# Kernel optimization log

Measured on AMD Instinct MI355X. Metric: run time of the kernel, lower is better.

The kernel has to match this reference:

```python
import jax, jax.numpy as jnp
import numpy as np

# --- model hyperparameters (from init_kwargs) ---
DIM = 2048
INTER = 1408          # moe_inter_dim
E = 16                # n_routed_experts
TOPK = 4              # n_activated_experts
G = 4                 # n_expert_groups
TOPK_G = 2            # n_limited_groups
N_SHARED = 2
ROUTE_SCALE = 1.0
INIT_STD = 0.02
B, S = 1, 2048


def setup_inputs() -> dict:
    key = jax.random.key(0)
    ks = jax.random.split(key, 9)
    std = INIT_STD
    x = jax.random.normal(ks[0], (B, S, DIM), jnp.float32)
    gate_w = jax.random.normal(ks[1], (E, DIM), jnp.float32) * std
    expert_bias = jnp.zeros((E,), jnp.float32)
    # stacked expert SwiGLU weights; torch Linear(in,out) -> stored here as [in,out]
    w1 = jax.random.normal(ks[2], (E, DIM, INTER), jnp.float32) * std
    w3 = jax.random.normal(ks[3], (E, DIM, INTER), jnp.float32) * std
    w2 = jax.random.normal(ks[4], (E, INTER, DIM), jnp.float32) * std
    # shared experts MLP (inter = n_shared_experts * moe_inter_dim)
    sh = N_SHARED * INTER
    sw1 = jax.random.normal(ks[5], (DIM, sh), jnp.float32) * std
    sw3 = jax.random.normal(ks[6], (DIM, sh), jnp.float32) * std
    sw2 = jax.random.normal(ks[7], (sh, DIM), jnp.float32) * std
    return {"x": x, "gate_w": gate_w, "expert_bias": expert_bias,
            "w1": w1, "w2": w2, "w3": w3,
            "sw1": sw1, "sw2": sw2, "sw3": sw3}


def reference(x, gate_w, expert_bias, w1, w2, w3, sw1, sw2, sw3):
    b, s, d = x.shape
    T = b * s
    xf = x.reshape(T, d)

    # ---- Gate ----
    scores = jax.nn.sigmoid(xf @ gate_w.T)          # [T, E] (score_function='sigmoid')
    original_scores = scores
    scores = scores + expert_bias
    # grouped routing: keep top-k groups, mask the rest to -inf
    sg = scores.reshape(T, G, E // G)
    group_scores = sg.max(axis=-1)                   # [T, G]
    _, gidx = jax.lax.top_k(group_scores, TOPK_G)    # [T, TOPK_G]
    gmask = jnp.zeros((T, G), bool).at[jnp.arange(T)[:, None], gidx].set(True)
    masked = jnp.where(gmask[:, :, None], sg, -jnp.inf).reshape(T, E)
    _, idx = jax.lax.top_k(masked, TOPK)             # [T, TOPK] expert indices
    w = jnp.take_along_axis(original_scores, idx, axis=1)
    w = w / jnp.sum(w, axis=-1, keepdims=True)       # sigmoid path normalization
    w = w * ROUTE_SCALE

    # dense combine weights: zero for non-selected experts -> exact same math
    cw = jnp.zeros((T, E), x.dtype).at[jnp.arange(T)[:, None], idx].add(w)

    # ---- routed experts (stacked SwiGLU) ----
    h = jax.nn.silu(jnp.einsum('td,edh->teh', xf, w1)) * jnp.einsum('td,edh->teh', xf, w3)
    y = jnp.einsum('teh,ehd,te->td', h, w2, cw)

    # ---- shared experts ----
    z = (jax.nn.silu(xf @ sw1) * (xf @ sw3)) @ sw2

    return (y + z).reshape(b, s, d)
```

## Files before the change

kernel.cpp:

```cpp
#include <hip/hip_runtime.h>
#include <hip/hip_bf16.h>

#define T_     2048
#define DIM_   2048
#define INTER_ 1408
#define SH_    2816
#define E_     16
#define TOPK_  4

typedef short bf16x8 __attribute__((ext_vector_type(8)));
typedef short bf16x4 __attribute__((ext_vector_type(4)));
typedef float f32x4  __attribute__((ext_vector_type(4)));

__device__ __forceinline__ short f2bf(float f) {
    unsigned u = __builtin_bit_cast(unsigned, f);
    u = (u + 0x7fffu + ((u >> 16) & 1u)) >> 16;
    return (short)u;
}
__device__ __forceinline__ float bf2f(short s) {
    unsigned u = ((unsigned)(unsigned short)s) << 16;
    return __builtin_bit_cast(float, u);
}
__device__ __forceinline__ f32x4 mfma16(bf16x8 a, bf16x8 b, f32x4 c) {
    return __builtin_amdgcn_mfma_f32_16x16x32_bf16(a, b, c, 0, 0, 0);
}

#define LDK 48
__device__ __forceinline__ int soff(int r, int slot) {
    return r * LDK + ((slot ^ ((r >> 2) & 3)) << 3);
}
__device__ __forceinline__ int qoff(int r, int slot) {
    return r * 32 + ((slot ^ ((r >> 1) & 3)) << 3);
}

__device__ __forceinline__ void async_copy16(short* lds, const short* g) {
#if defined(__has_builtin) && __has_builtin(__builtin_amdgcn_global_load_lds)
    __builtin_amdgcn_global_load_lds(
        (const __attribute__((address_space(1))) void*)g,
        (__attribute__((address_space(3))) void*)lds, 16, 0, 0);
#else
    *(bf16x8*)((char*)lds + (size_t)(threadIdx.x & 63) * 16) = *(const bf16x8*)g;
#endif
}

__device__ __forceinline__ bf16x8 pack44(float4 a, float4 b) {
    bf16x8 r;
    r[0] = f2bf(a.x); r[1] = f2bf(a.y); r[2] = f2bf(a.z); r[3] = f2bf(a.w);
    r[4] = f2bf(b.x); r[5] = f2bf(b.y); r[6] = f2bf(b.z); r[7] = f2bf(b.w);
    return r;
}

__global__ void zero_counts_kernel(int* __restrict__ counts) {
    if (threadIdx.x < E_) counts[threadIdx.x] = 0;
}

__global__ void transpose_bf16_kernel(const float* __restrict__ src,
                                      short* __restrict__ dst,
                                      int K, int N) {
    src += (size_t)blockIdx.z * K * N;
    dst += (size_t)blockIdx.z * N * K;
    int n0 = blockIdx.x * 64, k0 = blockIdx.y * 64;
    __shared__ short tile[64][66];
    int t = threadIdx.x;
    int hi = t >> 4;
    int c4 = (t & 15) << 2;
#pragma unroll
    for (int i = 0; i < 4; ++i) {
        int k = i * 16 + hi;
        float4 v = *(const float4*)(src + (size_t)(k0 + k) * N + n0 + c4);
        tile[k][c4 + 0] = f2bf(v.x);
        tile[k][c4 + 1] = f2bf(v.y);
        tile[k][c4 + 2] = f2bf(v.z);
        tile[k][c4 + 3] = f2bf(v.w);
    }
    __syncthreads();
#pragma unroll
    for (int i = 0; i < 4; ++i) {
        int n = i * 16 + hi;
        bf16x4 o;
        o[0] = tile[c4 + 0][n];
        o[1] = tile[c4 + 1][n];
        o[2] = tile[c4 + 2][n];
        o[3] = tile[c4 + 3][n];
        *(bf16x4*)(dst + (size_t)(n0 + n) * K + k0 + c4) = o;
    }
}

__global__ void gate_kernel(const float* __restrict__ X,
                            const float* __restrict__ GW,
                            const float* __restrict__ BIAS,
                            int*   __restrict__ counts,
                            int*   __restrict__ ltok,
                            int*   __restrict__ lslot,
                            float* __restrict__ lwt,
                            float* __restrict__ aw) {
    int t = blockIdx.x;
    int lane = threadIdx.x;
    const float* xp = X + (size_t)t * DIM_;
    float acc[E_];
#pragma unroll
    for (int e = 0; e < E_; ++e) acc[e] = 0.f;
    for (int d = lane; d < DIM_; d += 64) {
        float xv = xp[d];
#pragma unroll
        for (int e = 0; e < E_; ++e) acc[e] += xv * GW[e * DIM_ + d];
    }
#pragma unroll
    for (int off = 32; off > 0; off >>= 1) {
#pragma unroll
        for (int e = 0; e < E_; ++e) acc[e] += __shfl_down(acc[e], off, 64);
    }
    if (lane == 0) {
        float orig[E_], s[E_];
#pragma unroll
        for (int e = 0; e < E_; ++e) {
            float sg = 1.f / (1.f + expf(-acc[e]));
            orig[e] = sg;
            s[e] = sg + BIAS[e];
        }
        float gs[4];
#pragma unroll
        for (int g = 0; g < 4; ++g)
            gs[g] = fmaxf(fmaxf(s[4*g], s[4*g+1]), fmaxf(s[4*g+2], s[4*g+3]));
        int g0 = 0;
#pragma unroll
        for (int g = 1; g < 4; ++g) if (gs[g] > gs[g0]) g0 = g;
        int g1 = -1;
#pragma unroll
        for (int g = 0; g < 4; ++g)
            if (g != g0 && (g1 < 0 || gs[g] > gs[g1])) g1 = g;
        unsigned allow = (0xFu << (g0 * 4)) | (0xFu << (g1 * 4));
        unsigned taken = 0;
        int sel[TOPK_]; float wv[TOPK_]; float wsum = 0.f;
#pragma unroll
        for (int k = 0; k < TOPK_; ++k) {
            int bi = -1; float bv = 0.f;
#pragma unroll
            for (int e = 0; e < E_; ++e) {
                if (((allow >> e) & 1u) && !((taken >> e) & 1u)) {
                    if (bi < 0 || s[e] > bv) { bi = e; bv = s[e]; }
                }
            }
            taken |= 1u << bi;
            sel[k] = bi; wv[k] = orig[bi]; wsum += orig[bi];
        }
        float inv = 1.0f / wsum;
#pragma unroll
        for (int k = 0; k < TOPK_; ++k) {
            int e = sel[k];
            float w = wv[k] * inv;
            int pos = atomicAdd(&counts[e], 1);
            ltok [e * T_ + pos] = t;
            lslot[e * T_ + pos] = t * TOPK_ + k;
            lwt  [e * T_ + pos] = w;
            aw[t * TOPK_ + k] = w;
        }
    }
}

template<bool GATHER, bool BF16W>
__launch_bounds__(256, 2)
__global__ void swiglu_gemm(const float* __restrict__ X,
                            const void* __restrict__ W1g,
                            const void* __restrict__ W3g,
                            short* __restrict__ Hout,
                            int N, int K,
                            const int* __restrict__ counts,
                            const int* __restrict__ ltok,
                            const int* __restrict__ lslot) {
    int e = GATHER ? blockIdx.z : 0;
    int cnt = GATHER ? counts[e] : (int)(gridDim.y * 128);
    int row_base = blockIdx.y * 128;
    if (row_base >= cnt) return;
    int bn0 = blockIdx.x * 128;

    __shared__ __align__(16) short As [128 * LDK];
    __shared__ __align__(16) short Bs1[128 * LDK];
    __shared__ __align__(16) short Bs3[128 * LDK];

    int t = threadIdx.x;
    int ar = t >> 1, ah = t & 1;
    int arow = row_base + ar;
    bool avalid; int atok;
    if (GATHER) { avalid = arow < cnt; atok = avalid ? ltok[e * T_ + arow] : 0; }
    else        { avalid = true;       atok = arow; }
    const float* aptr = X + (size_t)atok * DIM_ + ah * 16;

    int l = t & 63, wv = t >> 6;
    int wm = (wv >> 1) << 6, wn = (wv & 1) << 6;
    int lr = l & 15, lk = l >> 4;

    const short* bSrc1[2]; const short* bSrc3[2];
    const float* Wf1 = nullptr; const float* Wf3 = nullptr;
    if constexpr (BF16W) {
        const short* Wb1 = (const short*)W1g + (size_t)e * N * K;
        const short* Wb3 = (const short*)W3g + (size_t)e * N * K;
        int r_ = l >> 2, sp = l & 3;
#pragma unroll
        for (int c = 0; c < 2; ++c) {
            int chunk = c * 4 + wv;
            int r = chunk * 16 + r_;
            int ss = sp ^ ((r >> 1) & 3);
            bSrc1[c] = Wb1 + (size_t)(bn0 + r) * K + ss * 8;
            bSrc3[c] = Wb3 + (size_t)(bn0 + r) * K + ss * 8;
        }
    } else {
        Wf1 = (const float*)W1g + (size_t)e * K * N;
        Wf3 = (const float*)W3g + (size_t)e * K * N;
    }

    f32x4 acc1[4][4], acc3[4][4];
    f32x4 z4 = {0.f, 0.f, 0.f, 0.f};
#pragma unroll
    for (int i = 0; i < 4; ++i)
#pragma unroll
        for (int j = 0; j < 4; ++j) { acc1[i][j] = z4; acc3[i][j] = z4; }

    for (int k0 = 0; k0 < K; k0 += 32) {
        float4 v0, v1, v2, v3;
        if (avalid) {
            const float4* p = (const float4*)(aptr + k0);
            v0 = p[0]; v1 = p[1]; v2 = p[2]; v3 = p[3];
        } else {
            v0 = v1 = v2 = v3 = make_float4(0.f, 0.f, 0.f, 0.f);
        }
        *(bf16x8*)&As[soff(ar, ah * 2)]     = pack44(v0, v1);
        *(bf16x8*)&As[soff(ar, ah * 2 + 1)] = pack44(v2, v3);
        if constexpr (BF16W) {
#pragma unroll
            for (int c = 0; c < 2; ++c) {
                int chunk = c * 4 + wv;
                async_copy16(&Bs1[chunk * 512], bSrc1[c] + k0);
                async_copy16(&Bs3[chunk * 512], bSrc3[c] + k0);
            }
        } else {
            for (int it = t; it < 512; it += 256) {
                int n = it & 127, kc = it >> 7;
                const float* b1p = Wf1 + (size_t)(k0 + kc * 8) * N + bn0 + n;
                const float* b3p = Wf3 + (size_t)(k0 + kc * 8) * N + bn0 + n;
                bf16x8 p1, p3;
#pragma unroll
                for (int j = 0; j < 8; ++j) {
                    p1[j] = f2bf(b1p[(size_t)j * N]);
                    p3[j] = f2bf(b3p[(size_t)j * N]);
                }
                *(bf16x8*)&Bs1[soff(n, kc)] = p1;
                *(bf16x8*)&Bs3[soff(n, kc)] = p3;
            }
        }
        __syncthreads();
        bf16x8 af[4], b1f[4], b3f[4];
#pragma unroll
        for (int mf = 0; mf < 4; ++mf)
            af[mf] = *(const bf16x8*)&As[soff(wm + mf * 16 + lr, lk)];
#pragma unroll
        for (int nf = 0; nf < 4; ++nf) {
            int n = wn + nf * 16 + lr;
            if constexpr (BF16W) {
                b1f[nf] = *(const bf16x8*)&Bs1[qoff(n, lk)];
                b3f[nf] = *(const bf16x8*)&Bs3[qoff(n, lk)];
            } else {
                b1f[nf] = *(const bf16x8*)&Bs1[soff(n, lk)];
                b3f[nf] = *(const bf16x8*)&Bs3[soff(n, lk)];
            }
        }
#pragma unroll
        for (int mf = 0; mf < 4; ++mf)
#pragma unroll
            for (int nf = 0; nf < 4; ++nf) {
                acc1[mf][nf] = mfma16(af[mf], b1f[nf], acc1[mf][nf]);
                acc3[mf][nf] = mfma16(af[mf], b3f[nf], acc3[mf][nf]);
            }
        __syncthreads();
    }
#pragma unroll
    for (int mf = 0; mf < 4; ++mf)
#pragma unroll
        for (int nf = 0; nf < 4; ++nf)
#pragma unroll
            for (int j = 0; j < 4; ++j) {
                float a1 = acc1[mf][nf][j];
                float a3 = acc3[mf][nf][j];
                float hv = a1 / (1.f + __expf(-a1)) * a3;
                int r = wm + mf * 16 + lk * 4 + j;
                int gr = row_base + r;
                int col = bn0 + wn + nf * 16 + lr;
                if (!GATHER || gr < cnt) {
                    size_t orow = GATHER ? (size_t)lslot[(size_t)e * T_ + gr]
                                         : (size_t)gr;
                    Hout[orow * (size_t)N + col] = f2bf(hv);
                }
            }
}

template<bool ROUTED, bool BF16W>
__launch_bounds__(256, 2)
__global__ void out_gemm(const short* __restrict__ Hg,
                         const void* __restrict__ W2g,
                         float* __restrict__ Out,
                         short* __restrict__ Obuf,
                         int K, int use_obuf,
                         const int* __restrict__ counts,
                         const int* __restrict__ lslot,
                         const float* __restrict__ lwt) {
    int e = ROUTED ? blockIdx.z : 0;
    int cnt = ROUTED ? counts[e] : T_;
    int row_base = blockIdx.y * 128;
    if (row_base >= cnt) return;
    int bn0 = blockIdx.x * 128;

    __shared__ __align__(16) short As[128 * LDK];
    __shared__ __align__(16) short Bs[128 * LDK];

    int t = threadIdx.x;
    int l = t & 63, wv = t >> 6;
    int wm = (wv >> 1) << 6, wn = (wv & 1) << 6;
    int lr = l & 15, lk = l >> 4;

    const short* aSrc[2]; const short* bSrc[2];
    const float* Wf2 = nullptr;
    const short* aptr = nullptr; bool avalid = true; int ar = 0, ah = 0;
    if constexpr (BF16W) {
        const short* Wb2 = (const short*)W2g + (size_t)e * (size_t)DIM_ * K;
        int r_ = l >> 2, sp = l & 3;
#pragma unroll
        for (int c = 0; c < 2; ++c) {
            int chunk = c * 4 + wv;
            int r = chunk * 16 + r_;
            int ss = sp ^ ((r >> 1) & 3);
            size_t hrow;
            if constexpr (ROUTED) {
                int gr = row_base + r;
                hrow = (size_t)((gr < cnt) ? lslot[(size_t)e * T_ + gr] : 0);
            } else {
                hrow = (size_t)(row_base + r);
            }
            aSrc[c] = Hg + hrow * K + ss * 8;
            bSrc[c] = Wb2 + (size_t)(bn0 + r) * K + ss * 8;
        }
    } else {
        Wf2 = (const float*)W2g + (size_t)e * K * DIM_;
        ar = t >> 1; ah = t & 1;
        int arow = row_base + ar;
        if constexpr (ROUTED) {
            avalid = arow < cnt;
            aptr = avalid ? Hg + (size_t)lslot[(size_t)e * T_ + arow] * K + ah * 16 : Hg;
        } else {
            aptr = Hg + (size_t)arow * K + ah * 16;
        }
    }

    f32x4 acc[4][4];
    f32x4 z4 = {0.f, 0.f, 0.f, 0.f};
#pragma unroll
    for (int i = 0; i < 4; ++i)
#pragma unroll
        for (int j = 0; j < 4; ++j) acc[i][j] = z4;

    for (int k0 = 0; k0 < K; k0 += 32) {
        if constexpr (BF16W) {
#pragma unroll
            for (int c = 0; c < 2; ++c) {
                int chunk = c * 4 + wv;
                async_copy16(&As[chunk * 512], aSrc[c] + k0);
                async_copy16(&Bs[chunk * 512], bSrc[c] + k0);
            }
        } else {
            bf16x8 pa0, pa1;
            if (avalid) {
                pa0 = *(const bf16x8*)(aptr + k0);
                pa1 = *(const bf16x8*)(aptr + k0 + 8);
            } else {
#pragma unroll
                for (int j = 0; j < 8; ++j) { pa0[j] = 0; pa1[j] = 0; }
            }
            *(bf16x8*)&As[soff(ar, ah * 2)]     = pa0;
            *(bf16x8*)&As[soff(ar, ah * 2 + 1)] = pa1;
            for (int it = t; it < 512; it += 256) {
                int n = it & 127, kc = it >> 7;
                const float* bp = Wf2 + (size_t)(k0 + kc * 8) * DIM_ + bn0 + n;
                bf16x8 p;
#pragma unroll
                for (int j = 0; j < 8; ++j) p[j] = f2bf(bp[(size_t)j * DIM_]);
                *(bf16x8*)&Bs[soff(n, kc)] = p;
            }
        }
        __syncthreads();
        bf16x8 af[4], bfr[4];
#pragma unroll
        for (int mf = 0; mf < 4; ++mf) {
            int r = wm + mf * 16 + lr;
            if constexpr (BF16W) af[mf] = *(const bf16x8*)&As[qoff(r, lk)];
            else                 af[mf] = *(const bf16x8*)&As[soff(r, lk)];
        }
#pragma unroll
        for (int nf = 0; nf < 4; ++nf) {
            int n = wn + nf * 16 + lr;
            if constexpr (BF16W) bfr[nf] = *(const bf16x8*)&Bs[qoff(n, lk)];
            else                 bfr[nf] = *(const bf16x8*)&Bs[soff(n, lk)];
        }
#pragma unroll
        for (int mf = 0; mf < 4; ++mf)
#pragma unroll
            for (int nf = 0; nf < 4; ++nf)
                acc[mf][nf] = mfma16(af[mf], bfr[nf], acc[mf][nf]);
        __syncthreads();
    }
#pragma unroll
    for (int mf = 0; mf < 4; ++mf)
#pragma unroll
        for (int nf = 0; nf < 4; ++nf)
#pragma unroll
            for (int j = 0; j < 4; ++j) {
                float v = acc[mf][nf][j];
                int r = wm + mf * 16 + lk * 4 + j;
                int gr = row_base + r;
                int col = bn0 + wn + nf * 16 + lr;
                if constexpr (ROUTED) {
                    if (gr < cnt) {
                        int a = lslot[(size_t)e * T_ + gr];
                        if (use_obuf) {
                            Obuf[(size_t)a * DIM_ + col] = f2bf(v);
                        } else {
                            float w = lwt[(size_t)e * T_ + gr];
                            atomicAdd(&Out[(size_t)(a >> 2) * DIM_ + col], v * w);
                        }
                    }
                } else {
                    Out[(size_t)gr * DIM_ + col] = v;
                }
            }
}

__global__ void combine_kernel(const short* __restrict__ Obuf,
                               const float* __restrict__ aw,
                               float* __restrict__ Out) {
    int t = blockIdx.x;
    int c0 = threadIdx.x << 3;
    float s[8];
#pragma unroll
    for (int j = 0; j < 8; ++j) s[j] = 0.f;
#pragma unroll
    for (int k = 0; k < TOPK_; ++k) {
        float w = aw[t * TOPK_ + k];
        const short* rp = Obuf + ((size_t)(t * TOPK_ + k)) * DIM_ + c0;
#pragma unroll
        for (int j = 0; j < 8; ++j) s[j] += w * bf2f(rp[j]);
    }
    float* op = Out + (size_t)t * DIM_ + c0;
#pragma unroll
    for (int j = 0; j < 8; ++j) op[j] += s[j];
}

extern "C" void kernel_launch(void* const* d_in, const int* in_sizes, int n_in,
                              void* d_out, int out_size, void* d_ws, size_t ws_size,
                              hipStream_t stream) {
    const float* x     = (const float*)d_in[0];
    const float* gw    = (const float*)d_in[1];
    const float* ebias = (const float*)d_in[2];
    const float* w1    = (const float*)d_in[3];
    const float* w2    = (const float*)d_in[4];
    const float* w3    = (const float*)d_in[5];
    const float* sw1   = (const float*)d_in[6];
    const float* sw2   = (const float*)d_in[7];
    const float* sw3   = (const float*)d_in[8];
    float* out = (float*)d_out;

    char* wsb = (char*)d_ws;
    int*   counts = (int*)wsb;
    int*   ltok   = (int*)(wsb + 1024);
    int*   lslot  = (int*)(wsb + 1024 + 131072);
    float* lwt    = (float*)(wsb + 1024 + 2 * 131072);
    float* aw     = (float*)(wsb + 1024 + 3 * 131072);
    size_t off = 1024 + 3 * 131072 + 32768;
    short* hbuf = (short*)(wsb + off);
    size_t hbuf_sz = (size_t)T_ * TOPK_ * INTER_ * 2;
    size_t obuf_sz = (size_t)T_ * TOPK_ * DIM_ * 2;
    size_t hs_sz   = (size_t)T_ * SH_ * 2;
    size_t wt_sz   = (size_t)E_ * INTER_ * DIM_ * 2;
    size_t swt_sz  = (size_t)SH_ * DIM_ * 2;

    size_t need_fp32a = off + hbuf_sz + hs_sz;
    size_t need_fp32  = need_fp32a + obuf_sz;
    size_t need_bf16  = need_fp32 + 3 * wt_sz + 3 * swt_sz;

    size_t o2 = off + hbuf_sz;
    short* obuf = (short*)(wsb + o2);
    int use_obuf = (ws_size >= need_fp32) ? 1 : 0;
    if (use_obuf) o2 += obuf_sz;
    short* hs = (short*)(wsb + o2); o2 += hs_sz;
    short* wt1  = (short*)(wsb + o2); o2 += wt_sz;
    short* wt3  = (short*)(wsb + o2); o2 += wt_sz;
    short* wt2  = (short*)(wsb + o2); o2 += wt_sz;
    short* swt1 = (short*)(wsb + o2); o2 += swt_sz;
    short* swt3 = (short*)(wsb + o2); o2 += swt_sz;
    short* swt2 = (short*)(wsb + o2);
    int bf16w = (ws_size >= need_bf16) ? 1 : 0;

    zero_counts_kernel<<<1, 64, 0, stream>>>(counts);
    gate_kernel<<<T_, 64, 0, stream>>>(x, gw, ebias, counts, ltok, lslot, lwt, aw);

    if (bf16w) {
        transpose_bf16_kernel<<<dim3(INTER_/64, DIM_/64, E_), 256, 0, stream>>>(w1, wt1, DIM_, INTER_);
        transpose_bf16_kernel<<<dim3(INTER_/64, DIM_/64, E_), 256, 0, stream>>>(w3, wt3, DIM_, INTER_);
        transpose_bf16_kernel<<<dim3(DIM_/64, INTER_/64, E_), 256, 0, stream>>>(w2, wt2, INTER_, DIM_);
        transpose_bf16_kernel<<<dim3(SH_/64, DIM_/64, 1), 256, 0, stream>>>(sw1, swt1, DIM_, SH_);
        transpose_bf16_kernel<<<dim3(SH_/64, DIM_/64, 1), 256, 0, stream>>>(sw3, swt3, DIM_, SH_);
        transpose_bf16_kernel<<<dim3(DIM_/64, SH_/64, 1), 256, 0, stream>>>(sw2, swt2, SH_, DIM_);

        swiglu_gemm<false, true><<<dim3(SH_/128, T_/128), 256, 0, stream>>>(
            x, swt1, swt3, hs, SH_, DIM_, nullptr, nullptr, nullptr);
        out_gemm<false, true><<<dim3(DIM_/128, T_/128), 256, 0, stream>>>(
            hs, swt2, out, nullptr, SH_, 0, nullptr, nullptr, nullptr);
        swiglu_gemm<true, true><<<dim3(INTER_/128, T_/128, E_), 256, 0, stream>>>(
            x, wt1, wt3, hbuf, INTER_, DIM_, counts, ltok, lslot);
        out_gemm<true, true><<<dim3(DIM_/128, T_/128, E_), 256, 0, stream>>>(
            hbuf, wt2, out, obuf, INTER_, 1, counts, lslot, lwt);
        combine_kernel<<<T_, 256, 0, stream>>>(obuf, aw, out);
    } else {
        swiglu_gemm<false, false><<<dim3(SH_/128, T_/128), 256, 0, stream>>>(
            x, sw1, sw3, hs, SH_, DIM_, nullptr, nullptr, nullptr);
        out_gemm<false, false><<<dim3(DIM_/128, T_/128), 256, 0, stream>>>(
            hs, sw2, out, nullptr, SH_, 0, nullptr, nullptr, nullptr);
        swiglu_gemm<true, false><<<dim3(INTER_/128, T_/128, E_), 256, 0, stream>>>(
            x, w1, w3, hbuf, INTER_, DIM_, counts, ltok, lslot);
        out_gemm<true, false><<<dim3(DIM_/128, T_/128, E_), 256, 0, stream>>>(
            hbuf, w2, out, obuf, INTER_, use_obuf, counts, lslot, lwt);
        if (use_obuf)
            combine_kernel<<<T_, 256, 0, stream>>>(obuf, aw, out);
    }
}
```

Before: 1.218 ms.

## Pre-convert activations to bf16, double-buffer async GEMM loads, fuse combine into shared GEMM

A separate kernel now converts x to bf16 once, so the SwiGLU GEMMs load A tiles with async global-to-LDS copies the same way they load weights. Both GEMMs now use double-buffered LDS with prefetch of the next K tile, which removes one barrier per iteration. The routed top-k combine moves into the shared-expert output GEMM epilogue, which drops combine_kernel and the read-modify-write of out. Other changes: the fp32-weight fallback path is removed, the transpose writes 16-byte vectors, out_gemm launch bounds go from 2 to 3, and the launches are reordered. The trade-off is that the code now always assumes a large enough workspace, and the larger LDS footprint may reduce occupancy.

```diff
diff --git a/kernel.cpp b/kernel.cpp
--- a/kernel.cpp
+++ b/kernel.cpp
@@ -24,25 +24,6 @@
 __device__ __forceinline__ f32x4 mfma16(bf16x8 a, bf16x8 b, f32x4 c) {
     return __builtin_amdgcn_mfma_f32_16x16x32_bf16(a, b, c, 0, 0, 0);
 }
-
-#define LDK 48
-__device__ __forceinline__ int soff(int r, int slot) {
-    return r * LDK + ((slot ^ ((r >> 2) & 3)) << 3);
-}
-__device__ __forceinline__ int qoff(int r, int slot) {
-    return r * 32 + ((slot ^ ((r >> 1) & 3)) << 3);
-}
-
-__device__ __forceinline__ void async_copy16(short* lds, const short* g) {
-#if defined(__has_builtin) && __has_builtin(__builtin_amdgcn_global_load_lds)
-    __builtin_amdgcn_global_load_lds(
-        (const __attribute__((address_space(1))) void*)g,
-        (__attribute__((address_space(3))) void*)lds, 16, 0, 0);
-#else
-    *(bf16x8*)((char*)lds + (size_t)(threadIdx.x & 63) * 16) = *(const bf16x8*)g;
-#endif
-}
-
 __device__ __forceinline__ bf16x8 pack44(float4 a, float4 b) {
     bf16x8 r;
     r[0] = f2bf(a.x); r[1] = f2bf(a.y); r[2] = f2bf(a.z); r[3] = f2bf(a.w);
@@ -50,8 +31,25 @@
     return r;
 }
 
+__device__ __forceinline__ int qoff(int r, int slot) {
+    return r * 32 + ((slot ^ ((r >> 1) & 3)) << 3);
+}
+
+__device__ __forceinline__ void async_copy16(short* lds, const short* g) {
+    __builtin_amdgcn_global_load_lds(
+        (const __attribute__((address_space(1))) void*)g,
+        (__attribute__((address_space(3))) void*)lds, 16, 0, 0);
+}
+
 __global__ void zero_counts_kernel(int* __restrict__ counts) {
     if (threadIdx.x < E_) counts[threadIdx.x] = 0;
+}
+
+__global__ void xconv_kernel(const float* __restrict__ x, short* __restrict__ xb) {
+    size_t i = ((size_t)blockIdx.x * 256 + threadIdx.x) * 8;
+    float4 a = *(const float4*)(x + i);
+    float4 b = *(const float4*)(x + i + 4);
+    *(bf16x8*)(xb + i) = pack44(a, b);
 }
 
 __global__ void transpose_bf16_kernel(const float* __restrict__ src,
@@ -74,15 +72,14 @@
         tile[k][c4 + 3] = f2bf(v.w);
     }
     __syncthreads();
-#pragma unroll
-    for (int i = 0; i < 4; ++i) {
-        int n = i * 16 + hi;
-        bf16x4 o;
-        o[0] = tile[c4 + 0][n];
-        o[1] = tile[c4 + 1][n];
-        o[2] = tile[c4 + 2][n];
-        o[3] = tile[c4 + 3][n];
-        *(bf16x4*)(dst + (size_t)(n0 + n) * K + k0 + c4) = o;
+    int n_ = t >> 3, kg = t & 7;
+#pragma unroll
+    for (int p = 0; p < 2; ++p) {
+        int n = p * 32 + n_;
+        bf16x8 o;
+#pragma unroll
+        for (int j = 0; j < 8; ++j) o[j] = tile[kg * 8 + j][n];
+        *(bf16x8*)(dst + (size_t)(n0 + n) * K + k0 + kg * 8) = o;
     }
 }
 
@@ -158,55 +155,48 @@
     }
 }
 
-template<bool GATHER, bool BF16W>
+template<bool GATHER>
 __launch_bounds__(256, 2)
-__global__ void swiglu_gemm(const float* __restrict__ X,
-                            const void* __restrict__ W1g,
-                            const void* __restrict__ W3g,
-                            short* __restrict__ Hout,
-                            int N, int K,
-                            const int* __restrict__ counts,
-                            const int* __restrict__ ltok,
-                            const int* __restrict__ lslot) {
+__global__ void swiglu_gemm2(const short* __restrict__ Xb,
+                             const short* __restrict__ W1g,
+                             const short* __restrict__ W3g,
+                             short* __restrict__ Hout,
+                             int N, int K,
+                             const int* __restrict__ counts,
+                             const int* __restrict__ ltok,
+                             const int* __restrict__ lslot) {
     int e = GATHER ? blockIdx.z : 0;
     int cnt = GATHER ? counts[e] : (int)(gridDim.y * 128);
     int row_base = blockIdx.y * 128;
     if (row_base >= cnt) return;
     int bn0 = blockIdx.x * 128;
-
-    __shared__ __align__(16) short As [128 * LDK];
-    __shared__ __align__(16) short Bs1[128 * LDK];
-    __shared__ __align__(16) short Bs3[128 * LDK];
-
-    int t = threadIdx.x;
-    int ar = t >> 1, ah = t & 1;
-    int arow = row_base + ar;
-    bool avalid; int atok;
-    if (GATHER) { avalid = arow < cnt; atok = avalid ? ltok[e * T_ + arow] : 0; }
-    else        { avalid = true;       atok = arow; }
-    const float* aptr = X + (size_t)atok * DIM_ + ah * 16;
-
-    int l = t & 63, wv = t >> 6;
+    const short* W1 = W1g + (size_t)e * N * K;
+    const short* W3 = W3g + (size_t)e * N * K;
+
+    __shared__ __align__(16) short As [2][4096];
+    __shared__ __align__(16) short Bs1[2][4096];
+    __shared__ __align__(16) short Bs3[2][4096];
+
+    int t = threadIdx.x, l = t & 63, wv = t >> 6;
     int wm = (wv >> 1) << 6, wn = (wv & 1) << 6;
     int lr = l & 15, lk = l >> 4;
-
-    const short* bSrc1[2]; const short* bSrc3[2];
-    const float* Wf1 = nullptr; const float* Wf3 = nullptr;
-    if constexpr (BF16W) {
-        const short* Wb1 = (const short*)W1g + (size_t)e * N * K;
-        const short* Wb3 = (const short*)W3g + (size_t)e * N * K;
-        int r_ = l >> 2, sp = l & 3;
-#pragma unroll
-        for (int c = 0; c < 2; ++c) {
-            int chunk = c * 4 + wv;
-            int r = chunk * 16 + r_;
-            int ss = sp ^ ((r >> 1) & 3);
-            bSrc1[c] = Wb1 + (size_t)(bn0 + r) * K + ss * 8;
-            bSrc3[c] = Wb3 + (size_t)(bn0 + r) * K + ss * 8;
-        }
-    } else {
-        Wf1 = (const float*)W1g + (size_t)e * K * N;
-        Wf3 = (const float*)W3g + (size_t)e * K * N;
+    int r_ = l >> 2, sp = l & 3;
+
+    const short *aS[2], *b1S[2], *b3S[2];
+#pragma unroll
+    for (int c = 0; c < 2; ++c) {
+        int chunk = c * 4 + wv;
+        int r = chunk * 16 + r_;
+        int ss = sp ^ ((r >> 1) & 3);
+        int grow = row_base + r;
+        int tok;
+        if constexpr (GATHER) {
+            int ci = grow < cnt ? grow : cnt - 1;
+            tok = ltok[e * T_ + ci];
+        } else tok = grow;
+        aS [c] = Xb + (size_t)tok * K + ss * 8;
+        b1S[c] = W1 + (size_t)(bn0 + r) * K + ss * 8;
+        b3S[c] = W3 + (size_t)(bn0 + r) * K + ss * 8;
     }
 
     f32x4 acc1[4][4], acc3[4][4];
@@ -216,53 +206,36 @@
 #pragma unroll
         for (int j = 0; j < 4; ++j) { acc1[i][j] = z4; acc3[i][j] = z4; }
 
-    for (int k0 = 0; k0 < K; k0 += 32) {
-        float4 v0, v1, v2, v3;
-        if (avalid) {
-            const float4* p = (const float4*)(aptr + k0);
-            v0 = p[0]; v1 = p[1]; v2 = p[2]; v3 = p[3];
-        } else {
-            v0 = v1 = v2 = v3 = make_float4(0.f, 0.f, 0.f, 0.f);
-        }
-        *(bf16x8*)&As[soff(ar, ah * 2)]     = pack44(v0, v1);
-        *(bf16x8*)&As[soff(ar, ah * 2 + 1)] = pack44(v2, v3);
-        if constexpr (BF16W) {
+    int nt = K >> 5;
+#pragma unroll
+    for (int c = 0; c < 2; ++c) {
+        int chunk = c * 4 + wv;
+        async_copy16(&As [0][chunk * 512], aS [c]);
+        async_copy16(&Bs1[0][chunk * 512], b1S[c]);
+        async_copy16(&Bs3[0][chunk * 512], b3S[c]);
+    }
+    __syncthreads();
+    int cur = 0;
+    for (int kt = 0; kt < nt; ++kt) {
+        if (kt + 1 < nt) {
+            int k0 = (kt + 1) << 5;
 #pragma unroll
             for (int c = 0; c < 2; ++c) {
                 int chunk = c * 4 + wv;
-                async_copy16(&Bs1[chunk * 512], bSrc1[c] + k0);
-                async_copy16(&Bs3[chunk * 512], bSrc3[c] + k0);
-            }
-        } else {
-            for (int it = t; it < 512; it += 256) {
-                int n = it & 127, kc = it >> 7;
-                const float* b1p = Wf1 + (size_t)(k0 + kc * 8) * N + bn0 + n;
-                const float* b3p = Wf3 + (size_t)(k0 + kc * 8) * N + bn0 + n;
-                bf16x8 p1, p3;
-#pragma unroll
-                for (int j = 0; j < 8; ++j) {
-                    p1[j] = f2bf(b1p[(size_t)j * N]);
-                    p3[j] = f2bf(b3p[(size_t)j * N]);
-                }
-                *(bf16x8*)&Bs1[soff(n, kc)] = p1;
-                *(bf16x8*)&Bs3[soff(n, kc)] = p3;
-            }
-        }
-        __syncthreads();
+                async_copy16(&As [cur ^ 1][chunk * 512], aS [c] + k0);
+                async_copy16(&Bs1[cur ^ 1][chunk * 512], b1S[c] + k0);
+                async_copy16(&Bs3[cur ^ 1][chunk * 512], b3S[c] + k0);
+            }
+        }
         bf16x8 af[4], b1f[4], b3f[4];
 #pragma unroll
         for (int mf = 0; mf < 4; ++mf)
-            af[mf] = *(const bf16x8*)&As[soff(wm + mf * 16 + lr, lk)];
+            af[mf] = *(const bf16x8*)&As[cur][qoff(wm + mf * 16 + lr, lk)];
 #pragma unroll
         for (int nf = 0; nf < 4; ++nf) {
             int n = wn + nf * 16 + lr;
-            if constexpr (BF16W) {
-                b1f[nf] = *(const bf16x8*)&Bs1[qoff(n, lk)];
-                b3f[nf] = *(const bf16x8*)&Bs3[qoff(n, lk)];
-            } else {
-                b1f[nf] = *(const bf16x8*)&Bs1[soff(n, lk)];
-                b3f[nf] = *(const bf16x8*)&Bs3[soff(n, lk)];
-            }
+            b1f[nf] = *(const bf16x8*)&Bs1[cur][qoff(n, lk)];
+            b3f[nf] = *(const bf16x8*)&Bs3[cur][qoff(n, lk)];
         }
 #pragma unroll
         for (int mf = 0; mf < 4; ++mf)
@@ -272,6 +245,7 @@
                 acc3[mf][nf] = mfma16(af[mf], b3f[nf], acc3[mf][nf]);
             }
         __syncthreads();
+        cur ^= 1;
     }
 #pragma unroll
     for (int mf = 0; mf < 4; ++mf)
@@ -293,61 +267,47 @@
             }
 }
 
-template<bool ROUTED, bool BF16W>
-__launch_bounds__(256, 2)
-__global__ void out_gemm(const short* __restrict__ Hg,
-                         const void* __restrict__ W2g,
-                         float* __restrict__ Out,
-                         short* __restrict__ Obuf,
-                         int K, int use_obuf,
-                         const int* __restrict__ counts,
-                         const int* __restrict__ lslot,
-                         const float* __restrict__ lwt) {
+template<bool ROUTED, bool COMBINE>
+__launch_bounds__(256, 3)
+__global__ void out_gemm2(const short* __restrict__ Hg,
+                          const short* __restrict__ W2g,
+                          float* __restrict__ Out,
+                          short* __restrict__ Obuf,
+                          const float* __restrict__ aw,
+                          int K,
+                          const int* __restrict__ counts,
+                          const int* __restrict__ lslot) {
     int e = ROUTED ? blockIdx.z : 0;
     int cnt = ROUTED ? counts[e] : T_;
     int row_base = blockIdx.y * 128;
     if (row_base >= cnt) return;
     int bn0 = blockIdx.x * 128;
-
-    __shared__ __align__(16) short As[128 * LDK];
-    __shared__ __align__(16) short Bs[128 * LDK];
-
-    int t = threadIdx.x;
-    int l = t & 63, wv = t >> 6;
+    const short* W2 = W2g + (size_t)e * (size_t)DIM_ * K;
+
+    __shared__ __align__(16) short As[2][4096];
+    __shared__ __align__(16) short Bs[2][4096];
+
+    int t = threadIdx.x, l = t & 63, wv = t >> 6;
     int wm = (wv >> 1) << 6, wn = (wv & 1) << 6;
     int lr = l & 15, lk = l >> 4;
-
-    const short* aSrc[2]; const short* bSrc[2];
-    const float* Wf2 = nullptr;
-    const short* aptr = nullptr; bool avalid = true; int ar = 0, ah = 0;
-    if constexpr (BF16W) {
-        const short* Wb2 = (const short*)W2g + (size_t)e * (size_t)DIM_ * K;
-        int r_ = l >> 2, sp = l & 3;
-#pragma unroll
-        for (int c = 0; c < 2; ++c) {
-            int chunk = c * 4 + wv;
-            int r = chunk * 16 + r_;
-            int ss = sp ^ ((r >> 1) & 3);
-            size_t hrow;
-            if constexpr (ROUTED) {
-                int gr = row_base + r;
-                hrow = (size_t)((gr < cnt) ? lslot[(size_t)e * T_ + gr] : 0);
-            } else {
-                hrow = (size_t)(row_base + r);
-            }
-            aSrc[c] = Hg + hrow * K + ss * 8;
-            bSrc[c] = Wb2 + (size_t)(bn0 + r) * K + ss * 8;
-        }
-    } else {
-        Wf2 = (const float*)W2g + (size_t)e * K * DIM_;
-        ar = t >> 1; ah = t & 1;
-        int arow = row_base + ar;
+    int r_ = l >> 2, sp = l & 3;
+
+    const short *aS[2], *bS[2];
+#pragma unroll
+    for (int c = 0; c < 2; ++c) {
+        int chunk = c * 4 + wv;
+        int r = chunk * 16 + r_;
+        int ss = sp ^ ((r >> 1) & 3);
+        size_t hrow;
         if constexpr (ROUTED) {
-            avalid = arow < cnt;
-            aptr = avalid ? Hg + (size_t)lslot[(size_t)e * T_ + arow] * K + ah * 16 : Hg;
+            int grow = row_base + r;
+            int ci = grow < cnt ? grow : cnt - 1;
+            hrow = (size_t)lslot[(size_t)e * T_ + ci];
         } else {
-            aptr = Hg + (size_t)arow * K + ah * 16;
-        }
+            hrow = (size_t)(row_base + r);
+        }
+        aS[c] = Hg + hrow * K + ss * 8;
+        bS[c] = W2 + (size_t)(bn0 + r) * K + ss * 8;
     }
 
     f32x4 acc[4][4];
@@ -357,54 +317,39 @@
 #pragma unroll
         for (int j = 0; j < 4; ++j) acc[i][j] = z4;
 
-    for (int k0 = 0; k0 < K; k0 += 32) {
-        if constexpr (BF16W) {
+    int nt = K >> 5;
+#pragma unroll
+    for (int c = 0; c < 2; ++c) {
+        int chunk = c * 4 + wv;
+        async_copy16(&As[0][chunk * 512], aS[c]);
+        async_copy16(&Bs[0][chunk * 512], bS[c]);
+    }
+    __syncthreads();
+    int cur = 0;
+    for (int kt = 0; kt < nt; ++kt) {
+        if (kt + 1 < nt) {
+            int k0 = (kt + 1) << 5;
 #pragma unroll
             for (int c = 0; c < 2; ++c) {
                 int chunk = c * 4 + wv;
-                async_copy16(&As[chunk * 512], aSrc[c] + k0);
-                async_copy16(&Bs[chunk * 512], bSrc[c] + k0);
-            }
-        } else {
-            bf16x8 pa0, pa1;
-            if (avalid) {
-                pa0 = *(const bf16x8*)(aptr + k0);
-                pa1 = *(const bf16x8*)(aptr + k0 + 8);
-            } else {
-#pragma unroll
-                for (int j = 0; j < 8; ++j) { pa0[j] = 0; pa1[j] = 0; }
-            }
-            *(bf16x8*)&As[soff(ar, ah * 2)]     = pa0;
-            *(bf16x8*)&As[soff(ar, ah * 2 + 1)] = pa1;
-            for (int it = t; it < 512; it += 256) {
-                int n = it & 127, kc = it >> 7;
-                const float* bp = Wf2 + (size_t)(k0 + kc * 8) * DIM_ + bn0 + n;
-                bf16x8 p;
-#pragma unroll
-                for (int j = 0; j < 8; ++j) p[j] = f2bf(bp[(size_t)j * DIM_]);
-                *(bf16x8*)&Bs[soff(n, kc)] = p;
-            }
-        }
-        __syncthreads();
+                async_copy16(&As[cur ^ 1][chunk * 512], aS[c] + k0);
+                async_copy16(&Bs[cur ^ 1][chunk * 512], bS[c] + k0);
+            }
+        }
         bf16x8 af[4], bfr[4];
 #pragma unroll
-        for (int mf = 0; mf < 4; ++mf) {
-            int r = wm + mf * 16 + lr;
-            if constexpr (BF16W) af[mf] = *(const bf16x8*)&As[qoff(r, lk)];
-            else                 af[mf] = *(const bf16x8*)&As[soff(r, lk)];
-        }
-#pragma unroll
-        for (int nf = 0; nf < 4; ++nf) {
-            int n = wn + nf * 16 + lr;
-            if constexpr (BF16W) bfr[nf] = *(const bf16x8*)&Bs[qoff(n, lk)];
-            else                 bfr[nf] = *(const bf16x8*)&Bs[soff(n, lk)];
-        }
+        for (int mf = 0; mf < 4; ++mf)
+            af[mf] = *(const bf16x8*)&As[cur][qoff(wm + mf * 16 + lr, lk)];
+#pragma unroll
+        for (int nf = 0; nf < 4; ++nf)
+            bfr[nf] = *(const bf16x8*)&Bs[cur][qoff(wn + nf * 16 + lr, lk)];
 #pragma unroll
         for (int mf = 0; mf < 4; ++mf)
 #pragma unroll
             for (int nf = 0; nf < 4; ++nf)
                 acc[mf][nf] = mfma16(af[mf], bfr[nf], acc[mf][nf]);
         __syncthreads();
+        cur ^= 1;
     }
 #pragma unroll
     for (int mf = 0; mf < 4; ++mf)
@@ -419,37 +364,20 @@
                 if constexpr (ROUTED) {
                     if (gr < cnt) {
                         int a = lslot[(size_t)e * T_ + gr];
-                        if (use_obuf) {
-                            Obuf[(size_t)a * DIM_ + col] = f2bf(v);
-                        } else {
-                            float w = lwt[(size_t)e * T_ + gr];
-                            atomicAdd(&Out[(size_t)(a >> 2) * DIM_ + col], v * w);
+                        Obuf[(size_t)a * DIM_ + col] = f2bf(v);
+                    }
+                } else {
+                    float o = v;
+                    if constexpr (COMBINE) {
+#pragma unroll
+                        for (int k = 0; k < TOPK_; ++k) {
+                            float w = aw[gr * TOPK_ + k];
+                            o += w * bf2f(Obuf[(size_t)(gr * TOPK_ + k) * DIM_ + col]);
                         }
                     }
-                } else {
-                    Out[(size_t)gr * DIM_ + col] = v;
+                    Out[(size_t)gr * DIM_ + col] = o;
                 }
             }
-}
-
-__global__ void combine_kernel(const short* __restrict__ Obuf,
-                               const float* __restrict__ aw,
-                               float* __restrict__ Out) {
-    int t = blockIdx.x;
-    int c0 = threadIdx.x << 3;
-    float s[8];
-#pragma unroll
-    for (int j = 0; j < 8; ++j) s[j] = 0.f;
-#pragma unroll
-    for (int k = 0; k < TOPK_; ++k) {
-        float w = aw[t * TOPK_ + k];
-        const short* rp = Obuf + ((size_t)(t * TOPK_ + k)) * DIM_ + c0;
-#pragma unroll
-        for (int j = 0; j < 8; ++j) s[j] += w * bf2f(rp[j]);
-    }
-    float* op = Out + (size_t)t * DIM_ + c0;
-#pragma unroll
-    for (int j = 0; j < 8; ++j) op[j] += s[j];
 }
 
 extern "C" void kernel_launch(void* const* d_in, const int* in_sizes, int n_in,
@@ -467,66 +395,40 @@
     float* out = (float*)d_out;
 
     char* wsb = (char*)d_ws;
-    int*   counts = (int*)wsb;
-    int*   ltok   = (int*)(wsb + 1024);
-    int*   lslot  = (int*)(wsb + 1024 + 131072);
-    float* lwt    = (float*)(wsb + 1024 + 2 * 131072);
-    float* aw     = (float*)(wsb + 1024 + 3 * 131072);
-    size_t off = 1024 + 3 * 131072 + 32768;
-    short* hbuf = (short*)(wsb + off);
-    size_t hbuf_sz = (size_t)T_ * TOPK_ * INTER_ * 2;
-    size_t obuf_sz = (size_t)T_ * TOPK_ * DIM_ * 2;
-    size_t hs_sz   = (size_t)T_ * SH_ * 2;
-    size_t wt_sz   = (size_t)E_ * INTER_ * DIM_ * 2;
-    size_t swt_sz  = (size_t)SH_ * DIM_ * 2;
-
-    size_t need_fp32a = off + hbuf_sz + hs_sz;
-    size_t need_fp32  = need_fp32a + obuf_sz;
-    size_t need_bf16  = need_fp32 + 3 * wt_sz + 3 * swt_sz;
-
-    size_t o2 = off + hbuf_sz;
-    short* obuf = (short*)(wsb + o2);
-    int use_obuf = (ws_size >= need_fp32) ? 1 : 0;
-    if (use_obuf) o2 += obuf_sz;
-    short* hs = (short*)(wsb + o2); o2 += hs_sz;
-    short* wt1  = (short*)(wsb + o2); o2 += wt_sz;
-    short* wt3  = (short*)(wsb + o2); o2 += wt_sz;
-    short* wt2  = (short*)(wsb + o2); o2 += wt_sz;
-    short* swt1 = (short*)(wsb + o2); o2 += swt_sz;
-    short* swt3 = (short*)(wsb + o2); o2 += swt_sz;
-    short* swt2 = (short*)(wsb + o2);
-    int bf16w = (ws_size >= need_bf16) ? 1 : 0;
+    size_t o = 0;
+    int*   counts = (int*)(wsb + o);  o += 1024;
+    int*   ltok   = (int*)(wsb + o);  o += 131072;
+    int*   lslot  = (int*)(wsb + o);  o += 131072;
+    float* lwt    = (float*)(wsb + o); o += 131072;
+    float* aw     = (float*)(wsb + o); o += 32768;
+    short* xb   = (short*)(wsb + o);  o += (size_t)T_ * DIM_ * 2;
+    short* hbuf = (short*)(wsb + o);  o += (size_t)T_ * TOPK_ * INTER_ * 2;
+    short* obuf = (short*)(wsb + o);  o += (size_t)T_ * TOPK_ * DIM_ * 2;
+    short* hs   = (short*)(wsb + o);  o += (size_t)T_ * SH_ * 2;
+    short* wt1  = (short*)(wsb + o);  o += (size_t)E_ * INTER_ * DIM_ * 2;
+    short* wt3  = (short*)(wsb + o);  o += (size_t)E_ * INTER_ * DIM_ * 2;
+    short* wt2  = (short*)(wsb + o);  o += (size_t)E_ * INTER_ * DIM_ * 2;
+    short* swt1 = (short*)(wsb + o);  o += (size_t)SH_ * DIM_ * 2;
+    short* swt3 = (short*)(wsb + o);  o += (size_t)SH_ * DIM_ * 2;
+    short* swt2 = (short*)(wsb + o);
 
     zero_counts_kernel<<<1, 64, 0, stream>>>(counts);
     gate_kernel<<<T_, 64, 0, stream>>>(x, gw, ebias, counts, ltok, lslot, lwt, aw);
-
-    if (bf16w) {
-        transpose_bf16_kernel<<<dim3(INTER_/64, DIM_/64, E_), 256, 0, stream>>>(w1, wt1, DIM_, INTER_);
-        transpose_bf16_kernel<<<dim3(INTER_/64, DIM_/64, E_), 256, 0, stream>>>(w3, wt3, DIM_, INTER_);
-        transpose_bf16_kernel<<<dim3(DIM_/64, INTER_/64, E_), 256, 0, stream>>>(w2, wt2, INTER_, DIM_);
-        transpose_bf16_kernel<<<dim3(SH_/64, DIM_/64, 1), 256, 0, stream>>>(sw1, swt1, DIM_, SH_);
-        transpose_bf16_kernel<<<dim3(SH_/64, DIM_/64, 1), 256, 0, stream>>>(sw3, swt3, DIM_, SH_);
-        transpose_bf16_kernel<<<dim3(DIM_/64, SH_/64, 1), 256, 0, stream>>>(sw2, swt2, SH_, DIM_);
-
-        swiglu_gemm<false, true><<<dim3(SH_/128, T_/128), 256, 0, stream>>>(
-            x, swt1, swt3, hs, SH_, DIM_, nullptr, nullptr, nullptr);
-        out_gemm<false, true><<<dim3(DIM_/128, T_/128), 256, 0, stream>>>(
-            hs, swt2, out, nullptr, SH_, 0, nullptr, nullptr, nullptr);
-        swiglu_gemm<true, true><<<dim3(INTER_/128, T_/128, E_), 256, 0, stream>>>(
-            x, wt1, wt3, hbuf, INTER_, DIM_, counts, ltok, lslot);
-        out_gemm<true, true><<<dim3(DIM_/128, T_/128, E_), 256, 0, stream>>>(
-            hbuf, wt2, out, obuf, INTER_, 1, counts, lslot, lwt);
-        combine_kernel<<<T_, 256, 0, stream>>>(obuf, aw, out);
-    } else {
-        swiglu_gemm<false, false><<<dim3(SH_/128, T_/128), 256, 0, stream>>>(
-            x, sw1, sw3, hs, SH_, DIM_, nullptr, nullptr, nullptr);
-        out_gemm<false, false><<<dim3(DIM_/128, T_/128), 256, 0, stream>>>(
-            hs, sw2, out, nullptr, SH_, 0, nullptr, nullptr, nullptr);
-        swiglu_gemm<true, false><<<dim3(INTER_/128, T_/128, E_), 256, 0, stream>>>(
-            x, w1, w3, hbuf, INTER_, DIM_, counts, ltok, lslot);
-        out_gemm<true, false><<<dim3(DIM_/128, T_/128, E_), 256, 0, stream>>>(
-            hbuf, w2, out, obuf, INTER_, use_obuf, counts, lslot, lwt);
-        if (use_obuf)
-            combine_kernel<<<T_, 256, 0, stream>>>(obuf, aw, out);
-    }
-}
+    xconv_kernel<<<(T_ * DIM_) / (256 * 8), 256, 0, stream>>>(x, xb);
+
+    transpose_bf16_kernel<<<dim3(INTER_/64, DIM_/64, E_), 256, 0, stream>>>(w1, wt1, DIM_, INTER_);
+    transpose_bf16_kernel<<<dim3(INTER_/64, DIM_/64, E_), 256, 0, stream>>>(w3, wt3, DIM_, INTER_);
+    swiglu_gemm2<true><<<dim3(INTER_/128, T_/128, E_), 256, 0, stream>>>(
+        xb, wt1, wt3, hbuf, INTER_, DIM_, counts, ltok, lslot);
+    transpose_bf16_kernel<<<dim3(DIM_/64, INTER_/64, E_), 256, 0, stream>>>(w2, wt2, INTER_, DIM_);
+    out_gemm2<true, false><<<dim3(DIM_/128, T_/128, E_), 256, 0, stream>>>(
+        hbuf, wt2, out, obuf, aw, INTER_, counts, lslot);
+
+    transpose_bf16_kernel<<<dim3(SH_/64, DIM_/64, 1), 256, 0, stream>>>(sw1, swt1, DIM_, SH_);
+    transpose_bf16_kernel<<<dim3(SH_/64, DIM_/64, 1), 256, 0, stream>>>(sw3, swt3, DIM_, SH_);
+    swiglu_gemm2<false><<<dim3(SH_/128, T_/128), 256, 0, stream>>>(
+        xb, swt1, swt3, hs, SH_, DIM_, nullptr, nullptr, nullptr);
+    transpose_bf16_kernel<<<dim3(DIM_/64, SH_/64, 1), 256, 0, stream>>>(sw2, swt2, SH_, DIM_);
+    out_gemm2<false, true><<<dim3(DIM_/128, T_/128), 256, 0, stream>>>(
+        hs, swt2, out, obuf, aw, SH_, nullptr, nullptr);
+}
```

Result: faster. 1.165 ms (-4.4%).
